# Kernel tuning notes

Measured on AMD Instinct MI355X. Metric: run time of the kernel, lower is better.

Reference implementation:

```python
import jax, jax.numpy as jnp
import numpy as np
from jax import lax

K = 5  # nearest neighbors (includes self)
EPS = 1e-6


def _relu(a):
    return jnp.maximum(a, 0.0)


def setup_inputs() -> dict:
    key = jax.random.key(0)
    ks = jax.random.split(key, 16)
    B, N, D = 8, 4096, 2
    LD = 64  # local_dim

    def w(k, fan_in, fan_out):
        return jax.random.normal(k, (fan_in, fan_out), jnp.float32) / np.sqrt(fan_in)

    x = jax.random.normal(ks[0], (B, N, D), jnp.float32)
    inp = {
        "x": x,
        # local_mlp: D->64->128->LD
        "lw1": w(ks[1], D, 64), "lb1": jnp.zeros((64,), jnp.float32),
        "lw2": w(ks[2], 64, 128), "lb2": jnp.zeros((128,), jnp.float32),
        "lw3": w(ks[3], 128, LD), "lb3": jnp.zeros((LD,), jnp.float32),
        # cls_branch: (D+LD)->128->128
        "cw1": w(ks[4], D + LD, 128), "cb1": jnp.zeros((128,), jnp.float32),
        "cw2": w(ks[5], 128, 128), "cb2": jnp.zeros((128,), jnp.float32),
        # topo_branch: LD->128->128
        "tw1": w(ks[6], LD, 128), "tb1": jnp.zeros((128,), jnp.float32),
        "tw2": w(ks[7], 128, 128), "tb2": jnp.zeros((128,), jnp.float32),
    }
    return inp


def reference(x, lw1, lb1, lw2, lb2, lw3, lb3,
              cw1, cb1, cw2, cb2, tw1, tb1, tw2, tb2):
    B, N, D = x.shape
    # squared pairwise distances (B,N,N)
    sq = jnp.sum(x * x, axis=-1)
    dist_sq = sq[:, :, None] + sq[:, None, :] - 2.0 * jnp.einsum("bnd,bmd->bnm", x, x)
    _, idx = lax.top_k(-dist_sq, K)  # (B,N,K) nearest (self first)

    neighbors = x[jnp.arange(B)[:, None, None], idx]          # (B,N,K,D)
    rel = neighbors - x[:, :, None, :]                         # relative coords
    centered = rel - rel.mean(axis=2, keepdims=True)           # (B,N,K,D)
    cov = jnp.einsum("bnki,bnkj->bnij", centered, centered) / (K - 1)

    e, v = jnp.linalg.eigh(cov + EPS * jnp.eye(2, dtype=x.dtype))  # ascending eigvals
    v1 = v[..., :, 1]                                          # principal eigenvector
    base_angle = jnp.arctan2(v1[..., 1], v1[..., 0])[..., None]  # (B,N,1)

    base_axes = jnp.sqrt(jnp.maximum(e, EPS))                  # (B,N,2)
    base_axes = base_axes[..., ::-1]                           # descending: major first
    base_axes = base_axes / (base_axes.max(axis=-1, keepdims=True) + EPS)
    base_axes = jnp.maximum(base_axes, 0.2)

    lcc = jnp.einsum("bnki,bnij->bnkj", centered, v)           # canonical coords
    h = _relu(lcc @ lw1 + lb1)
    h = _relu(h @ lw2 + lb2)
    h = _relu(h @ lw3 + lb3)                                   # (B,N,K,LD)
    local_feats = h.max(axis=2)                                # (B,N,LD)

    cls_in = jnp.concatenate([x, local_feats], axis=-1)
    cls_features = _relu(_relu(cls_in @ cw1 + cb1) @ cw2 + cb2)
    topo_features = _relu(_relu(local_feats @ tw1 + tb1) @ tw2 + tb2)
    return (cls_features, topo_features, base_angle, base_axes)
```

## Files before the change

kernel.cpp:

```cpp
#include <hip/hip_runtime.h>
#include <math.h>

#pragma clang fp contract(off)

#define NPTS 4096
#define PTS  32768
#define ROWS 163840
#define QN   8
#define QLEN 512
#define SLOTS 8

#define EPS_L   5.9604644775390625e-8f
#define EPS2_L  3.5527136788005009e-15f
#define SAFMIN_L 1.1754943508222875e-38f

__device__ __forceinline__ float frn_mul(float a, float b) { float r = a * b; return r; }
__device__ __forceinline__ float frn_add(float a, float b) { float r = a + b; return r; }
__device__ __forceinline__ float frn_sub(float a, float b) { float r = a - b; return r; }
__device__ __forceinline__ float frn_div(float a, float b) { float r = a / b; return r; }

__device__ __forceinline__ float ref_sq(float x0, float x1) {
  return frn_add(frn_mul(x0, x0), frn_mul(x1, x1));
}
__device__ __forceinline__ float ref_key(float nx, float ny, float sqn,
                                         float mx, float my, float sqm) {
  float dot = fmaf(ny, my, frn_mul(nx, mx));
  float s = frn_add(sqn, sqm);
  return fmaf(-2.0f, dot, s);
}

__global__ __launch_bounds__(256) void prep_w(
    const float* __restrict__ lw1, const float* __restrict__ lw2, const float* __restrict__ lw3,
    const float* __restrict__ cw1, const float* __restrict__ cw2,
    const float* __restrict__ tw1, const float* __restrict__ tw2,
    float* __restrict__ wt) {
  const int Ks[7]   = {2, 64, 128, 66, 128, 64, 128};
  const int Kp[7]   = {2, 64, 128, 80, 128, 64, 128};
  const int Ns[7]   = {64, 128, 64, 128, 128, 128, 128};
  const int offs[7] = {0, 128, 8320, 16512, 26752, 43136, 51328};
  const float* srcs[7] = {lw1, lw2, lw3, cw1, cw2, tw1, tw2};
  int b = blockIdx.x;
  const float* src = srcs[b];
  float* dst = wt + offs[b];
  int K = Ks[b], KP = Kp[b], N = Ns[b];
  for (int e = threadIdx.x; e < KP * N; e += 256) {
    int j = e / KP, i = e - j * KP;
    dst[e] = (i < K) ? src[i * N + j] : 0.0f;
  }
}

__device__ __forceinline__ void cand_step(float mex, float mey, float cx, float cy,
                                          unsigned int idx, unsigned int T,
                                          unsigned int* sbuf, int t,
                                          unsigned int& cnt) {
  float dx = mex - cx, dy = mey - cy;
  float dist = fmaf(dy, dy, dx * dx);
  unsigned int v = (__float_as_uint(dist) & 0xFFFFF000u) | idx;
  sbuf[cnt * 128 + t] = v;
  cnt += (v < T) ? 1u : 0u;
}

__global__ __launch_bounds__(128) void knn_scan(const float* __restrict__ x,
                                                unsigned int* __restrict__ ipart) {
  __shared__ float2 cand[QLEN];
  __shared__ unsigned int sbuf[16 * 128];
  int bx = blockIdx.x;
  int q = bx & (QN - 1);
  int pg = bx >> 3;
  int batch = pg >> 5;
  const float* xb = x + (size_t)batch * NPTS * 2;
  int c0 = q * QLEN;
  for (int i = threadIdx.x; i < QLEN; i += 128)
    cand[i] = ((const float2*)xb)[c0 + i];
  __syncthreads();
  int t = threadIdx.x;
  int p = pg * 128 + t;
  float2 me = ((const float2*)x)[p];
  unsigned int d[SLOTS];
#pragma unroll
  for (int s = 0; s < SLOTS; s++) d[s] = 0xFFFFFFFFu;
  unsigned int T = 0xFFFFFFFFu;
  unsigned int cnt = 0;
  for (int mm = 0; mm < QLEN / 4; mm++) {
    float4 c01 = ((const float4*)cand)[2 * mm];
    float4 c23 = ((const float4*)cand)[2 * mm + 1];
    unsigned int idx0 = (unsigned int)(c0 + 4 * mm);
    cand_step(me.x, me.y, c01.x, c01.y, idx0 + 0u, T, sbuf, t, cnt);
    cand_step(me.x, me.y, c01.z, c01.w, idx0 + 1u, T, sbuf, t, cnt);
    cand_step(me.x, me.y, c23.x, c23.y, idx0 + 2u, T, sbuf, t, cnt);
    cand_step(me.x, me.y, c23.z, c23.w, idx0 + 3u, T, sbuf, t, cnt);
    if (__any((int)(cnt >= 13u))) {
#pragma unroll
      for (int j = 0; j < 16; j++) {
        unsigned int u = ((unsigned)j < cnt) ? sbuf[j * 128 + t] : 0xFFFFFFFFu;
#pragma unroll
        for (int s = 0; s < SLOTS; s++) {
          unsigned int lo = min(u, d[s]);
          unsigned int hi = max(u, d[s]);
          d[s] = lo; u = hi;
        }
      }
      cnt = 0;
      T = d[SLOTS - 1];
    }
  }
#pragma unroll
  for (int j = 0; j < 16; j++) {
    unsigned int u = ((unsigned)j < cnt) ? sbuf[j * 128 + t] : 0xFFFFFFFFu;
#pragma unroll
    for (int s = 0; s < SLOTS; s++) {
      unsigned int lo = min(u, d[s]);
      unsigned int hi = max(u, d[s]);
      d[s] = lo; u = hi;
    }
  }
#pragma unroll
  for (int s = 0; s < SLOTS; s++)
    ipart[((size_t)(q * SLOTS + s)) * PTS + p] = d[s];
}

__global__ __launch_bounds__(128) void merge_geom(const float* __restrict__ x,
    const unsigned int* __restrict__ ipart,
    float2* __restrict__ lcct2,
    float* __restrict__ angle_out, float2* __restrict__ axes_out,
    float* __restrict__ lftx) {
  int p = blockIdx.x * 128 + threadIdx.x;
  int batch = p >> 12;
  const float2* xb = (const float2*)(x + (size_t)batch * NPTS * 2);
  float2 me = ((const float2*)x)[p];
  lftx[p] = me.x;
  lftx[PTS + p] = me.y;
#pragma unroll
  for (int r = 66; r < 80; r++) lftx[(size_t)r * PTS + p] = 0.0f;
  float sqn = ref_sq(me.x, me.y);

  unsigned int g[SLOTS];
#pragma unroll
  for (int s = 0; s < SLOTS; s++) g[s] = 0xFFFFFFFFu;
  for (int qs = 0; qs < QN * SLOTS; qs++) {
    unsigned int v = ipart[(size_t)qs * PTS + p];
#pragma unroll
    for (int s = 0; s < SLOTS; s++) {
      unsigned int lo = min(v, g[s]);
      unsigned int hi = max(v, g[s]);
      g[s] = lo; v = hi;
    }
  }
  float dk[5]; int id[5];
#pragma unroll
  for (int s = 0; s < 5; s++) { dk[s] = 3.0e38f; id[s] = 0x7fffffff; }
#pragma unroll
  for (int s8 = 0; s8 < SLOTS; s8++) {
    int ci = (int)(g[s8] & 0xFFFu);
    float2 c = xb[ci];
    float key = ref_key(me.x, me.y, sqn, c.x, c.y, ref_sq(c.x, c.y));
    float v = key; int vi = ci;
#pragma unroll
    for (int s = 0; s < 5; s++) {
      bool lt = (v < dk[s]) || (v == dk[s] && vi < id[s]);
      float tv = dk[s]; int ti = id[s];
      if (lt) { dk[s] = v; id[s] = vi; v = tv; vi = ti; }
    }
  }
  float rx[5], ry[5];
  float sx = 0.f, sy = 0.f;
#pragma unroll
  for (int k = 0; k < 5; k++) {
    float2 nb = xb[id[k]];
    rx[k] = frn_sub(nb.x, me.x); ry[k] = frn_sub(nb.y, me.y);
    sx = frn_add(sx, rx[k]); sy = frn_add(sy, ry[k]);
  }
  float mx = frn_div(sx, 5.0f), my = frn_div(sy, 5.0f);
  float c00 = 0.f, c01 = 0.f, c11 = 0.f;
#pragma unroll
  for (int k = 0; k < 5; k++) {
    rx[k] = frn_sub(rx[k], mx); ry[k] = frn_sub(ry[k], my);
    c00 = frn_add(c00, frn_mul(rx[k], rx[k]));
    c01 = frn_add(c01, frn_mul(rx[k], ry[k]));
    c11 = frn_add(c11, frn_mul(ry[k], ry[k]));
  }
  c00 = frn_div(c00, 4.0f); c01 = frn_div(c01, 4.0f); c11 = frn_div(c11, 4.0f);
  float A = frn_add(c00, 1e-6f), Bv = c01, C = frn_add(c11, 1e-6f);

  float absA = fabsf(A), absC = fabsf(C), absB = fabsf(Bv);
  float thr = frn_mul(frn_mul(sqrtf(absA), sqrtf(absC)), EPS_L);
  bool diag = (absB == 0.f) || (absB <= thr);
  if (!diag) {
    bool qr = (absC < absA);
    float b2 = frn_mul(absB, absB);
    float t = qr ? frn_add(frn_mul(frn_mul(EPS2_L, absC), absA), SAFMIN_L)
                 : frn_add(frn_mul(frn_mul(EPS2_L, absA), absC), SAFMIN_L);
    if (b2 <= t) diag = true;
  }
  float e1, e2, v00, v10, v01, v11;
  if (diag) {
    if (C < A) { e1 = C; e2 = A; v00 = 0.f; v10 = 1.f; v01 = 1.f; v11 = 0.f; }
    else       { e1 = A; e2 = C; v00 = 1.f; v10 = 0.f; v01 = 0.f; v11 = 1.f; }
  } else {
    float sm = frn_add(A, C), df = frn_sub(A, C);
    float adf = fabsf(df), tb = frn_add(Bv, Bv), ab = fabsf(tb);
    float rt;
    if (adf > ab) {
      float r = frn_div(ab, adf);
      rt = frn_mul(adf, sqrtf(frn_add(1.0f, frn_mul(r, r))));
    } else if (adf < ab) {
      float r = frn_div(adf, ab);
      rt = frn_mul(ab, sqrtf(frn_add(1.0f, frn_mul(r, r))));
    } else {
      rt = frn_mul(ab, sqrtf(2.0f));
    }
    float acmx, acmn;
    if (absA > absC) { acmx = A; acmn = C; } else { acmx = C; acmn = A; }
    float rt1, rt2; int sgn1;
    if (sm < 0.f) {
      rt1 = frn_mul(0.5f, frn_sub(sm, rt)); sgn1 = -1;
      rt2 = frn_sub(frn_mul(frn_div(acmx, rt1), acmn), frn_mul(frn_div(Bv, rt1), Bv));
    } else if (sm > 0.f) {
      rt1 = frn_mul(0.5f, frn_add(sm, rt)); sgn1 = 1;
      rt2 = frn_sub(frn_mul(frn_div(acmx, rt1), acmn), frn_mul(frn_div(Bv, rt1), Bv));
    } else {
      rt1 = frn_mul(0.5f, rt); rt2 = frn_mul(-0.5f, rt); sgn1 = 1;
    }
    float cs, cs1, sn1; int sgn2;
    if (df >= 0.f) { cs = frn_add(df, rt); sgn2 = 1; }
    else           { cs = frn_sub(df, rt); sgn2 = -1; }
    float acs = fabsf(cs);
    if (acs > ab) {
      float ct = frn_div(-tb, cs);
      sn1 = frn_div(1.0f, sqrtf(frn_add(1.0f, frn_mul(ct, ct))));
      cs1 = frn_mul(ct, sn1);
    } else {
      if (ab == 0.f) { cs1 = 1.0f; sn1 = 0.0f; }
      else {
        float tn = frn_div(-cs, tb);
        cs1 = frn_div(1.0f, sqrtf(frn_add(1.0f, frn_mul(tn, tn))));
        sn1 = frn_mul(tn, cs1);
      }
    }
    if (sgn1 == sgn2) { float t = cs1; cs1 = -sn1; sn1 = t; }
    if (rt2 < rt1) { e1 = rt2; e2 = rt1; v00 = -sn1; v10 = cs1; v01 = cs1;  v11 = sn1; }
    else           { e1 = rt1; e2 = rt2; v00 = cs1;  v10 = sn1; v01 = -sn1; v11 = cs1; }
  }

  angle_out[p] = atan2f(v11, v01);
  float aM = sqrtf(fmaxf(e2, 1e-6f));
  float am = sqrtf(fmaxf(e1, 1e-6f));
  float den = frn_add(fmaxf(aM, am), 1e-6f);
  axes_out[p] = make_float2(fmaxf(frn_div(aM, den), 0.2f),
                            fmaxf(frn_div(am, den), 0.2f));

  size_t rowb = (size_t)p * 5;
#pragma unroll
  for (int k = 0; k < 5; k++) {
    float l0 = frn_add(frn_mul(rx[k], v00), frn_mul(ry[k], v10));
    float l1 = frn_add(frn_mul(rx[k], v01), frn_mul(ry[k], v11));
    lcct2[rowb + k] = make_float2(l0, l1);
  }
}

__global__ __launch_bounds__(256, 3) void gemm_l2(
    const float2* __restrict__ lcct2, const float* __restrict__ lw1t,
    const float* __restrict__ lb1,
    const float* __restrict__ wt, const float* __restrict__ bias,
    float* __restrict__ out_t, int M) {
  __shared__ float alds[16 * 128];
  __shared__ float wlds[16 * 128];
  __shared__ float w1s[192];
  int t = threadIdx.x;
  int m0 = blockIdx.x * 128;
  if (t < 192) w1s[t] = (t < 128) ? lw1t[t] : lb1[t - 128];
  int mloc = t & 127;
  int kbase = t >> 7;
  float2 lme = lcct2[m0 + mloc];
  int tm = t & 15;
  int tn = t >> 4;
  float acc[8][8];
#pragma unroll
  for (int j = 0; j < 8; j++) {
    float b = bias[tn * 8 + j];
#pragma unroll
    for (int i = 0; i < 8; i++) acc[j][i] = b;
  }
  for (int kt = 0; kt < 4; kt++) {
    int k0 = kt * 16;
    __syncthreads();
#pragma unroll
    for (int pp = 0; pp < 8; pp++) {
      int kk = pp * 2 + kbase;
      int k = k0 + kk;
      float h = fmaf(lme.y, w1s[2 * k + 1], fmaf(lme.x, w1s[2 * k], w1s[128 + k]));
      alds[kk * 128 + mloc] = fmaxf(h, 0.f);
    }
#pragma unroll
    for (int pp = 0; pp < 2; pp++) {
      int e = pp * 256 + t;
      int n = e >> 2;
      int kc = e & 3;
      float4 v = *(const float4*)(wt + (size_t)n * 64 + k0 + kc * 4);
      wlds[(kc * 4 + 0) * 128 + n] = v.x;
      wlds[(kc * 4 + 1) * 128 + n] = v.y;
      wlds[(kc * 4 + 2) * 128 + n] = v.z;
      wlds[(kc * 4 + 3) * 128 + n] = v.w;
    }
    __syncthreads();
#pragma unroll
    for (int kk = 0; kk < 16; kk++) {
      float af[8], wf[8];
      *(float4*)(af)     = *(const float4*)(alds + kk * 128 + tm * 8);
      *(float4*)(af + 4) = *(const float4*)(alds + kk * 128 + tm * 8 + 4);
      *(float4*)(wf)     = *(const float4*)(wlds + kk * 128 + tn * 8);
      *(float4*)(wf + 4) = *(const float4*)(wlds + kk * 128 + tn * 8 + 4);
#pragma unroll
      for (int j = 0; j < 8; j++)
#pragma unroll
        for (int i = 0; i < 8; i++)
          acc[j][i] = fmaf(af[i], wf[j], acc[j][i]);
    }
  }
#pragma unroll
  for (int j = 0; j < 8; j++) {
    int n = tn * 8 + j;
    float4 o0, o1;
    o0.x = fmaxf(acc[j][0], 0.f); o0.y = fmaxf(acc[j][1], 0.f);
    o0.z = fmaxf(acc[j][2], 0.f); o0.w = fmaxf(acc[j][3], 0.f);
    o1.x = fmaxf(acc[j][4], 0.f); o1.y = fmaxf(acc[j][5], 0.f);
    o1.z = fmaxf(acc[j][6], 0.f); o1.w = fmaxf(acc[j][7], 0.f);
    float* dst = out_t + (size_t)n * M + m0 + tm * 8;
    *(float4*)(dst) = o0;
    *(float4*)(dst + 4) = o1;
  }
}

__global__ __launch_bounds__(512, 4) void gemm_l3max(
    const float* __restrict__ h2, const float* __restrict__ wt,
    const float* __restrict__ bias, float* __restrict__ lftx) {
  __shared__ float alds[16 * 320];
  __shared__ float wlds[16 * 64];
  int t = threadIdx.x;
  int m0 = blockIdx.x * 320;
  int pt = t & 63;
  int ng = t >> 6;
  float acc[5][8];
#pragma unroll
  for (int j = 0; j < 8; j++) {
    float b = bias[ng * 8 + j];
#pragma unroll
    for (int r = 0; r < 5; r++) acc[r][j] = b;
  }
  for (int kt = 0; kt < 8; kt++) {
    int k0 = kt * 16;
    __syncthreads();
    for (int e = t; e < 1280; e += 512) {
      int kk = e / 80;
      int m4 = e - kk * 80;
      float4 v = *(const float4*)(h2 + (size_t)(k0 + kk) * ROWS + m0 + m4 * 4);
      *(float4*)(alds + kk * 320 + m4 * 4) = v;
    }
    if (t < 256) {
      int n = t >> 2, kc = t & 3;
      float4 v = *(const float4*)(wt + (size_t)n * 128 + k0 + kc * 4);
      wlds[(kc * 4 + 0) * 64 + n] = v.x;
      wlds[(kc * 4 + 1) * 64 + n] = v.y;
      wlds[(kc * 4 + 2) * 64 + n] = v.z;
      wlds[(kc * 4 + 3) * 64 + n] = v.w;
    }
    __syncthreads();
#pragma unroll
    for (int kk = 0; kk < 16; kk++) {
      float af[5], wf[8];
#pragma unroll
      for (int r = 0; r < 5; r++) af[r] = alds[kk * 320 + pt * 5 + r];
      *(float4*)(wf)     = *(const float4*)(wlds + kk * 64 + ng * 8);
      *(float4*)(wf + 4) = *(const float4*)(wlds + kk * 64 + ng * 8 + 4);
#pragma unroll
      for (int r = 0; r < 5; r++)
#pragma unroll
        for (int j = 0; j < 8; j++)
          acc[r][j] = fmaf(af[r], wf[j], acc[r][j]);
    }
  }
  int p = blockIdx.x * 64 + pt;
#pragma unroll
  for (int j = 0; j < 8; j++) {
    float r0 = fmaxf(acc[0][j], 0.f), r1 = fmaxf(acc[1][j], 0.f);
    float r2 = fmaxf(acc[2][j], 0.f), r3 = fmaxf(acc[3][j], 0.f);
    float r4 = fmaxf(acc[4][j], 0.f);
    float m = fmaxf(fmaxf(fmaxf(r0, r1), fmaxf(r2, r3)), r4);
    lftx[(size_t)(ng * 8 + j + 2) * PTS + p] = m;
  }
}

__global__ __launch_bounds__(256, 3) void gemm_head1(
    const float* __restrict__ lftx, const float* __restrict__ wtbase,
    const float* __restrict__ cb1, const float* __restrict__ tb1,
    float* __restrict__ a1c, float* __restrict__ a1t) {
  __shared__ float alds[16 * 128];
  __shared__ float wlds[16 * 128];
  int bid = blockIdx.x;
  bool isC = bid < 256;
  const float* in_t = isC ? lftx : (lftx + 2 * PTS);
  const float* wt   = isC ? (wtbase + 16512) : (wtbase + 43136);
  const float* bias = isC ? cb1 : tb1;
  float* out_t      = isC ? a1c : a1t;
  int Kstr = isC ? 80 : 64;
  int KT   = isC ? 5 : 4;
  int m0 = (bid & 255) * 128;
  int t = threadIdx.x;
  int tm = t & 15;
  int tn = t >> 4;
  float acc[8][8];
#pragma unroll
  for (int j = 0; j < 8; j++) {
    float b = bias[tn * 8 + j];
#pragma unroll
    for (int i = 0; i < 8; i++) acc[j][i] = b;
  }
  for (int kt = 0; kt < KT; kt++) {
    int k0 = kt * 16;
    __syncthreads();
#pragma unroll
    for (int pp = 0; pp < 2; pp++) {
      int e = pp * 256 + t;
      int kk = e >> 5;
      int m4 = e & 31;
      float4 v = *(const float4*)(in_t + (size_t)(k0 + kk) * PTS + m0 + m4 * 4);
      *(float4*)(alds + kk * 128 + m4 * 4) = v;
    }
#pragma unroll
    for (int pp = 0; pp < 2; pp++) {
      int e = pp * 256 + t;
      int n = e >> 2;
      int kc = e & 3;
      float4 v = *(const float4*)(wt + (size_t)n * Kstr + k0 + kc * 4);
      wlds[(kc * 4 + 0) * 128 + n] = v.x;
      wlds[(kc * 4 + 1) * 128 + n] = v.y;
      wlds[(kc * 4 + 2) * 128 + n] = v.z;
      wlds[(kc * 4 + 3) * 128 + n] = v.w;
    }
    __syncthreads();
#pragma unroll
    for (int kk = 0; kk < 16; kk++) {
      float af[8], wf[8];
      *(float4*)(af)     = *(const float4*)(alds + kk * 128 + tm * 8);
      *(float4*)(af + 4) = *(const float4*)(alds + kk * 128 + tm * 8 + 4);
      *(float4*)(wf)     = *(const float4*)(wlds + kk * 128 + tn * 8);
      *(float4*)(wf + 4) = *(const float4*)(wlds + kk * 128 + tn * 8 + 4);
#pragma unroll
      for (int j = 0; j < 8; j++)
#pragma unroll
        for (int i = 0; i < 8; i++)
          acc[j][i] = fmaf(af[i], wf[j], acc[j][i]);
    }
  }
#pragma unroll
  for (int j = 0; j < 8; j++) {
    int n = tn * 8 + j;
    float4 o0, o1;
    o0.x = fmaxf(acc[j][0], 0.f); o0.y = fmaxf(acc[j][1], 0.f);
    o0.z = fmaxf(acc[j][2], 0.f); o0.w = fmaxf(acc[j][3], 0.f);
    o1.x = fmaxf(acc[j][4], 0.f); o1.y = fmaxf(acc[j][5], 0.f);
    o1.z = fmaxf(acc[j][6], 0.f); o1.w = fmaxf(acc[j][7], 0.f);
    float* dst = out_t + (size_t)n * PTS + m0 + tm * 8;
    *(float4*)(dst) = o0;
    *(float4*)(dst + 4) = o1;
  }
}

__global__ __launch_bounds__(256, 3) void gemm_head2(
    const float* __restrict__ a1c, const float* __restrict__ a1t,
    const float* __restrict__ wtbase,
    const float* __restrict__ cb2, const float* __restrict__ tb2,
    float* __restrict__ outbase) {
  __shared__ float alds[16 * 128];
  __shared__ float wlds[16 * 128];
  int bid = blockIdx.x;
  bool isC = bid < 256;
  const float* in_t = isC ? a1c : a1t;
  const float* wt   = isC ? (wtbase + 26752) : (wtbase + 51328);
  const float* bias = isC ? cb2 : tb2;
  float* out        = isC ? outbase : (outbase + 4194304);
  int m0 = (bid & 255) * 128;
  int t = threadIdx.x;
  int tm = t & 15;
  int tn = t >> 4;
  float acc[8][8];
#pragma unroll
  for (int j = 0; j < 8; j++) {
    float b = bias[tn * 8 + j];
#pragma unroll
    for (int i = 0; i < 8; i++) acc[j][i] = b;
  }
  for (int kt = 0; kt < 8; kt++) {
    int k0 = kt * 16;
    __syncthreads();
#pragma unroll
    for (int pp = 0; pp < 2; pp++) {
      int e = pp * 256 + t;
      int kk = e >> 5;
      int m4 = e & 31;
      float4 v = *(const float4*)(in_t + (size_t)(k0 + kk) * PTS + m0 + m4 * 4);
      *(float4*)(alds + kk * 128 + m4 * 4) = v;
    }
#pragma unroll
    for (int pp = 0; pp < 2; pp++) {
      int e = pp * 256 + t;
      int n = e >> 2;
      int kc = e & 3;
      float4 v = *(const float4*)(wt + (size_t)n * 128 + k0 + kc * 4);
      wlds[(kc * 4 + 0) * 128 + n] = v.x;
      wlds[(kc * 4 + 1) * 128 + n] = v.y;
      wlds[(kc * 4 + 2) * 128 + n] = v.z;
      wlds[(kc * 4 + 3) * 128 + n] = v.w;
    }
    __syncthreads();
#pragma unroll
    for (int kk = 0; kk < 16; kk++) {
      float af[8], wf[8];
      *(float4*)(af)     = *(const float4*)(alds + kk * 128 + tm * 8);
      *(float4*)(af + 4) = *(const float4*)(alds + kk * 128 + tm * 8 + 4);
      *(float4*)(wf)     = *(const float4*)(wlds + kk * 128 + tn * 8);
      *(float4*)(wf + 4) = *(const float4*)(wlds + kk * 128 + tn * 8 + 4);
#pragma unroll
      for (int j = 0; j < 8; j++)
#pragma unroll
        for (int i = 0; i < 8; i++)
          acc[j][i] = fmaf(af[i], wf[j], acc[j][i]);
    }
  }
#pragma unroll
  for (int i = 0; i < 8; i++) {
    int m = m0 + tm * 8 + i;
    float4 o0, o1;
    o0.x = fmaxf(acc[0][i], 0.f); o0.y = fmaxf(acc[1][i], 0.f);
    o0.z = fmaxf(acc[2][i], 0.f); o0.w = fmaxf(acc[3][i], 0.f);
    o1.x = fmaxf(acc[4][i], 0.f); o1.y = fmaxf(acc[5][i], 0.f);
    o1.z = fmaxf(acc[6][i], 0.f); o1.w = fmaxf(acc[7][i], 0.f);
    float* dst = out + (size_t)m * 128 + tn * 8;
    *(float4*)(dst) = o0;
    *(float4*)(dst + 4) = o1;
  }
}

extern "C" void kernel_launch(void* const* d_in, const int* in_sizes, int n_in,
                              void* d_out, int out_size, void* d_ws, size_t ws_size,
                              hipStream_t stream) {
  const float* x   = (const float*)d_in[0];
  const float* lb1 = (const float*)d_in[2];
  const float* lb2 = (const float*)d_in[4];
  const float* lb3 = (const float*)d_in[6];
  const float* cb1 = (const float*)d_in[8];
  const float* cb2 = (const float*)d_in[10];
  const float* tb1 = (const float*)d_in[12];
  const float* tb2 = (const float*)d_in[14];

  float* out = (float*)d_out;
  float* angle_out = out + 8388608;
  float* axes_out  = out + 8421376;

  float* W = (float*)d_ws;
  float* wt    = W;
  float* R1    = W + 67712;
  float* R2    = R1 + 10485760;
  float* R3    = R2 + 10485760;
  float* lftx  = R3 + 20971520;
  float* lcct2 = lftx + 2621440;
  unsigned int* ipart = (unsigned int*)R1;
  float* a1c   = R2;
  float* a1t   = R2 + 4194304;
  float* h2    = R3;

  prep_w<<<7, 256, 0, stream>>>((const float*)d_in[1], (const float*)d_in[3], (const float*)d_in[5],
                                (const float*)d_in[7], (const float*)d_in[9],
                                (const float*)d_in[11], (const float*)d_in[13], wt);
  knn_scan<<<2048, 128, 0, stream>>>(x, ipart);
  merge_geom<<<256, 128, 0, stream>>>(x, ipart, (float2*)lcct2, angle_out, (float2*)axes_out, lftx);

  gemm_l2<<<ROWS / 128, 256, 0, stream>>>((const float2*)lcct2, wt + 0, lb1,
                                          wt + 128, lb2, h2, ROWS);
  gemm_l3max<<<PTS / 64, 512, 0, stream>>>(h2, wt + 8320, lb3, lftx);

  gemm_head1<<<512, 256, 0, stream>>>(lftx, wt, cb1, tb1, a1c, a1t);
  gemm_head2<<<512, 256, 0, stream>>>(a1c, a1t, wt, cb2, tb2, out);
}
```

Baseline: 301.8 us.

## Fuse head GEMM layers via LDS and use bitonic merge in kNN merge

The two head MLP GEMMs are fused into one kernel: the first layer's 128x128 activation tile is kept in a 64KB LDS buffer and consumed directly by the second layer. This removes the global write and re-read of the intermediate activations and one kernel launch. The LDS footprint grows and the occupancy hint is dropped, so fewer blocks may fit per CU. Separately, the top-8 merge in merge_geom replaces 64 sequential insertion steps with 7 bitonic-style merges of sorted 8-element lists, cutting min/max operations.

```diff
diff --git a/kernel.cpp b/kernel.cpp
--- a/kernel.cpp
+++ b/kernel.cpp
@@ -119,6 +119,8 @@
     ipart[((size_t)(q * SLOTS + s)) * PTS + p] = d[s];
 }
 
+#define CAS(a, b) { unsigned int _l = min(a, b), _h = max(a, b); a = _l; b = _h; }
+
 __global__ __launch_bounds__(128) void merge_geom(const float* __restrict__ x,
     const unsigned int* __restrict__ ipart,
     float2* __restrict__ lcct2,
@@ -136,16 +138,21 @@
 
   unsigned int g[SLOTS];
 #pragma unroll
-  for (int s = 0; s < SLOTS; s++) g[s] = 0xFFFFFFFFu;
-  for (int qs = 0; qs < QN * SLOTS; qs++) {
-    unsigned int v = ipart[(size_t)qs * PTS + p];
-#pragma unroll
-    for (int s = 0; s < SLOTS; s++) {
-      unsigned int lo = min(v, g[s]);
-      unsigned int hi = max(v, g[s]);
-      g[s] = lo; v = hi;
-    }
-  }
+  for (int s = 0; s < SLOTS; s++) g[s] = ipart[(size_t)s * PTS + p];
+  for (int qs = 1; qs < QN; qs++) {
+    unsigned int B[SLOTS];
+#pragma unroll
+    for (int s = 0; s < SLOTS; s++) B[s] = ipart[(size_t)(qs * SLOTS + s) * PTS + p];
+    unsigned int w[SLOTS];
+#pragma unroll
+    for (int s = 0; s < SLOTS; s++) w[s] = min(g[s], B[SLOTS - 1 - s]);
+    CAS(w[0], w[4]); CAS(w[1], w[5]); CAS(w[2], w[6]); CAS(w[3], w[7]);
+    CAS(w[0], w[2]); CAS(w[1], w[3]); CAS(w[4], w[6]); CAS(w[5], w[7]);
+    CAS(w[0], w[1]); CAS(w[2], w[3]); CAS(w[4], w[5]); CAS(w[6], w[7]);
+#pragma unroll
+    for (int s = 0; s < SLOTS; s++) g[s] = w[s];
+  }
+
   float dk[5]; int id[5];
 #pragma unroll
   for (int s = 0; s < 5; s++) { dk[s] = 3.0e38f; id[s] = 0x7fffffff; }
@@ -390,18 +397,22 @@
   }
 }
 
-__global__ __launch_bounds__(256, 3) void gemm_head1(
+__global__ __launch_bounds__(256) void gemm_head(
     const float* __restrict__ lftx, const float* __restrict__ wtbase,
     const float* __restrict__ cb1, const float* __restrict__ tb1,
-    float* __restrict__ a1c, float* __restrict__ a1t) {
+    const float* __restrict__ cb2, const float* __restrict__ tb2,
+    float* __restrict__ outbase) {
+  __shared__ float a1lds[128 * 128];
   __shared__ float alds[16 * 128];
   __shared__ float wlds[16 * 128];
   int bid = blockIdx.x;
   bool isC = bid < 256;
   const float* in_t = isC ? lftx : (lftx + 2 * PTS);
-  const float* wt   = isC ? (wtbase + 16512) : (wtbase + 43136);
-  const float* bias = isC ? cb1 : tb1;
-  float* out_t      = isC ? a1c : a1t;
+  const float* w1   = isC ? (wtbase + 16512) : (wtbase + 43136);
+  const float* b1   = isC ? cb1 : tb1;
+  const float* w2   = isC ? (wtbase + 26752) : (wtbase + 51328);
+  const float* b2   = isC ? cb2 : tb2;
+  float* out        = isC ? outbase : (outbase + 4194304);
   int Kstr = isC ? 80 : 64;
   int KT   = isC ? 5 : 4;
   int m0 = (bid & 255) * 128;
@@ -409,9 +420,10 @@
   int tm = t & 15;
   int tn = t >> 4;
   float acc[8][8];
-#pragma unroll
-  for (int j = 0; j < 8; j++) {
-    float b = bias[tn * 8 + j];
+
+#pragma unroll
+  for (int j = 0; j < 8; j++) {
+    float b = b1[tn * 8 + j];
 #pragma unroll
     for (int i = 0; i < 8; i++) acc[j][i] = b;
   }
@@ -431,7 +443,7 @@
       int e = pp * 256 + t;
       int n = e >> 2;
       int kc = e & 3;
-      float4 v = *(const float4*)(wt + (size_t)n * Kstr + k0 + kc * 4);
+      float4 v = *(const float4*)(w1 + (size_t)n * Kstr + k0 + kc * 4);
       wlds[(kc * 4 + 0) * 128 + n] = v.x;
       wlds[(kc * 4 + 1) * 128 + n] = v.y;
       wlds[(kc * 4 + 2) * 128 + n] = v.z;
@@ -460,53 +472,25 @@
     o0.z = fmaxf(acc[j][2], 0.f); o0.w = fmaxf(acc[j][3], 0.f);
     o1.x = fmaxf(acc[j][4], 0.f); o1.y = fmaxf(acc[j][5], 0.f);
     o1.z = fmaxf(acc[j][6], 0.f); o1.w = fmaxf(acc[j][7], 0.f);
-    float* dst = out_t + (size_t)n * PTS + m0 + tm * 8;
-    *(float4*)(dst) = o0;
-    *(float4*)(dst + 4) = o1;
-  }
-}
-
-__global__ __launch_bounds__(256, 3) void gemm_head2(
-    const float* __restrict__ a1c, const float* __restrict__ a1t,
-    const float* __restrict__ wtbase,
-    const float* __restrict__ cb2, const float* __restrict__ tb2,
-    float* __restrict__ outbase) {
-  __shared__ float alds[16 * 128];
-  __shared__ float wlds[16 * 128];
-  int bid = blockIdx.x;
-  bool isC = bid < 256;
-  const float* in_t = isC ? a1c : a1t;
-  const float* wt   = isC ? (wtbase + 26752) : (wtbase + 51328);
-  const float* bias = isC ? cb2 : tb2;
-  float* out        = isC ? outbase : (outbase + 4194304);
-  int m0 = (bid & 255) * 128;
-  int t = threadIdx.x;
-  int tm = t & 15;
-  int tn = t >> 4;
-  float acc[8][8];
-#pragma unroll
-  for (int j = 0; j < 8; j++) {
-    float b = bias[tn * 8 + j];
+    *(float4*)(a1lds + n * 128 + tm * 8)     = o0;
+    *(float4*)(a1lds + n * 128 + tm * 8 + 4) = o1;
+  }
+
+#pragma unroll
+  for (int j = 0; j < 8; j++) {
+    float b = b2[tn * 8 + j];
 #pragma unroll
     for (int i = 0; i < 8; i++) acc[j][i] = b;
   }
   for (int kt = 0; kt < 8; kt++) {
     int k0 = kt * 16;
     __syncthreads();
-#pragma unroll
-    for (int pp = 0; pp < 2; pp++) {
-      int e = pp * 256 + t;
-      int kk = e >> 5;
-      int m4 = e & 31;
-      float4 v = *(const float4*)(in_t + (size_t)(k0 + kk) * PTS + m0 + m4 * 4);
-      *(float4*)(alds + kk * 128 + m4 * 4) = v;
-    }
 #pragma unroll
     for (int pp = 0; pp < 2; pp++) {
       int e = pp * 256 + t;
       int n = e >> 2;
       int kc = e & 3;
-      float4 v = *(const float4*)(wt + (size_t)n * 128 + k0 + kc * 4);
+      float4 v = *(const float4*)(w2 + (size_t)n * 128 + k0 + kc * 4);
       wlds[(kc * 4 + 0) * 128 + n] = v.x;
       wlds[(kc * 4 + 1) * 128 + n] = v.y;
       wlds[(kc * 4 + 2) * 128 + n] = v.z;
@@ -516,8 +500,8 @@
 #pragma unroll
     for (int kk = 0; kk < 16; kk++) {
       float af[8], wf[8];
-      *(float4*)(af)     = *(const float4*)(alds + kk * 128 + tm * 8);
-      *(float4*)(af + 4) = *(const float4*)(alds + kk * 128 + tm * 8 + 4);
+      *(float4*)(af)     = *(const float4*)(a1lds + (k0 + kk) * 128 + tm * 8);
+      *(float4*)(af + 4) = *(const float4*)(a1lds + (k0 + kk) * 128 + tm * 8 + 4);
       *(float4*)(wf)     = *(const float4*)(wlds + kk * 128 + tn * 8);
       *(float4*)(wf + 4) = *(const float4*)(wlds + kk * 128 + tn * 8 + 4);
 #pragma unroll
@@ -565,9 +549,8 @@
   float* lftx  = R3 + 20971520;
   float* lcct2 = lftx + 2621440;
   unsigned int* ipart = (unsigned int*)R1;
-  float* a1c   = R2;
-  float* a1t   = R2 + 4194304;
   float* h2    = R3;
+  (void)R2;
 
   prep_w<<<7, 256, 0, stream>>>((const float*)d_in[1], (const float*)d_in[3], (const float*)d_in[5],
                                 (const float*)d_in[7], (const float*)d_in[9],
@@ -579,6 +562,5 @@
                                           wt + 128, lb2, h2, ROWS);
   gemm_l3max<<<PTS / 64, 512, 0, stream>>>(h2, wt + 8320, lb3, lftx);
 
-  gemm_head1<<<512, 256, 0, stream>>>(lftx, wt, cb1, tb1, a1c, a1t);
-  gemm_head2<<<512, 256, 0, stream>>>(a1c, a1t, wt, cb2, tb2, out);
-}
+  gemm_head<<<512, 256, 0, stream>>>(lftx, wt, cb1, tb1, cb2, tb2, out);
+}
```

New measurement: 300.6 us. About the same (-0.4%).
